# Performance work log

Measured on AMD Instinct MI355X. Metric: run time of the kernel, lower is better.

The kernel has to match this reference:

```python
import jax, jax.numpy as jnp
from jax import lax
import numpy as np

D_MODEL = 512
D_STATE = 16
D_CONV = 4
EXPAND = 2
D_INNER = EXPAND * D_MODEL
DT_RANK = (D_MODEL + 15) // 16  # ceil(d_model/16) = 32
B, L = 4, 1024


def setup_inputs() -> dict:
    key = jax.random.key(0)
    ks = jax.random.split(key, 12)
    s = 0.02
    inp = {
        "feature": jax.random.normal(ks[0], (B, L, D_MODEL), jnp.float32),
        "ln_w": jnp.ones((D_MODEL,), jnp.float32),
        "ln_b": jnp.zeros((D_MODEL,), jnp.float32),
        "in_proj_w": jax.random.normal(ks[1], (2 * D_INNER, D_MODEL), jnp.float32) * s,
        "conv_w": jax.random.normal(ks[2], (D_INNER, D_CONV), jnp.float32) * 0.1,
        "conv_b": jnp.zeros((D_INNER,), jnp.float32),
        "x_proj_w": jax.random.normal(ks[3], (DT_RANK + 2 * D_STATE, D_INNER), jnp.float32) * s,
        "dt_proj_w": jax.random.normal(ks[4], (D_INNER, DT_RANK), jnp.float32) * 0.1,
        "dt_proj_b": jax.random.normal(ks[5], (D_INNER,), jnp.float32) * 0.1 - 4.0,
        "A_log": jnp.log(jnp.broadcast_to(jnp.arange(1, D_STATE + 1, dtype=jnp.float32), (D_INNER, D_STATE))),
        "D": jnp.ones((D_INNER,), jnp.float32),
        "out_proj_w": jax.random.normal(ks[6], (D_MODEL, D_INNER), jnp.float32) * s,
    }
    return inp


def _mamba_block(xn, in_proj_w, conv_w, conv_b, x_proj_w, dt_proj_w, dt_proj_b, A_log, D, out_proj_w):
    # xn: [B, L, d_model]
    xz = jnp.einsum('bld,ed->ble', xn, in_proj_w)          # [B, L, 2*d_inner]
    x, z = xz[..., :D_INNER], xz[..., D_INNER:]
    # causal depthwise conv along L
    xc = jnp.transpose(x, (0, 2, 1))                        # [B, d_inner, L]
    xc = lax.conv_general_dilated(
        xc, conv_w[:, None, :], (1,), [(D_CONV - 1, 0)],
        feature_group_count=D_INNER,
        dimension_numbers=('NCH', 'OIH', 'NCH')) + conv_b[None, :, None]
    x = jax.nn.silu(jnp.transpose(xc, (0, 2, 1)))           # [B, L, d_inner]
    x_dbl = jnp.einsum('bld,ed->ble', x, x_proj_w)          # [B, L, dt_rank+2*d_state]
    dt = x_dbl[..., :DT_RANK]
    Bm = x_dbl[..., DT_RANK:DT_RANK + D_STATE]
    Cm = x_dbl[..., DT_RANK + D_STATE:]
    dt = jax.nn.softplus(jnp.einsum('blr,dr->bld', dt, dt_proj_w) + dt_proj_b)  # [B,L,d_inner]
    A = -jnp.exp(A_log)                                     # [d_inner, d_state]

    def step(h, inp):
        dt_t, B_t, C_t, x_t = inp                           # [B,d_inner],[B,d_state],[B,d_state],[B,d_inner]
        dA = jnp.exp(dt_t[..., None] * A)                   # [B, d_inner, d_state]
        h = dA * h + (dt_t * x_t)[..., None] * B_t[:, None, :]
        y = jnp.einsum('bds,bs->bd', h, C_t)
        return h, y

    xs = (jnp.transpose(dt, (1, 0, 2)), jnp.transpose(Bm, (1, 0, 2)),
          jnp.transpose(Cm, (1, 0, 2)), jnp.transpose(x, (1, 0, 2)))
    h0 = jnp.zeros((xn.shape[0], D_INNER, D_STATE), xn.dtype)
    _, ys = lax.scan(step, h0, xs)                          # ys: [L, B, d_inner]
    y = jnp.transpose(ys, (1, 0, 2)) + x * D
    y = y * jax.nn.silu(z)
    return jnp.einsum('bld,ed->ble', y, out_proj_w)         # [B, L, d_model]


def reference(feature, ln_w, ln_b, in_proj_w, conv_w, conv_b, x_proj_w,
              dt_proj_w, dt_proj_b, A_log, D, out_proj_w):
    eps = 1e-5
    mu = jnp.mean(feature, axis=-1, keepdims=True)
    var = jnp.var(feature, axis=-1, keepdims=True)
    xn = (feature - mu) / jnp.sqrt(var + eps) * ln_w + ln_b
    out = _mamba_block(xn, in_proj_w, conv_w, conv_b, x_proj_w,
                       dt_proj_w, dt_proj_b, A_log, D, out_proj_w)
    return xn + out
```

## Files before the change

kernel.cpp:

```cpp
#include <hip/hip_runtime.h>
#include <hip/hip_bf16.h>
#include <math.h>

#define B_SZ 4
#define L_SZ 1024
#define DM   512
#define DI   1024
#define DS   16
#define DTR  32
#define NXD  64
#define M_ROWS (B_SZ*L_SZ)
#define CHK  64
#define CLEN 16
#define NCH  (B_SZ*DI)
#define PLANE (NCH*DS)
#define LDA  40
#define KSPL 8

typedef __attribute__((ext_vector_type(8))) short short8;
typedef __attribute__((ext_vector_type(4))) float f32x4;
typedef __hip_bfloat16 bf16;

__device__ __forceinline__ float bf2f(bf16 x){ return __bfloat162float(x); }
__device__ __forceinline__ float fsig(float x){ return __builtin_amdgcn_rcpf(1.f + __expf(-x)); }
__device__ __forceinline__ unsigned short bfbits(float x){ bf16 b = __float2bfloat16(x); return *(unsigned short*)&b; }
#define LOG2E 1.44269504f

__device__ __forceinline__ bool is_f32(const void* lnw){
    return *(const unsigned*)lnw == 0x3F800000u;
}
__device__ __forceinline__ float loadf(const void* s, int i, bool f){
    return f ? ((const float*)s)[i] : bf2f(((const bf16*)s)[i]);
}
__device__ __forceinline__ bf16 loadb(const void* s, int i, bool f){
    return f ? __float2bfloat16(((const float*)s)[i]) : ((const bf16*)s)[i];
}

#define CVT_TOTAL 1694720
__global__ __launch_bounds__(256) void prep_kernel(
        const void* __restrict__ feat, const void* __restrict__ lnw, const void* __restrict__ lnb,
        const void* __restrict__ w_in, const void* __restrict__ w_x, const void* __restrict__ w_out,
        const void* __restrict__ w_dt, const void* __restrict__ b_dt,
        const void* __restrict__ alog, const void* __restrict__ dvec,
        const void* __restrict__ cw, const void* __restrict__ cb,
        bf16* __restrict__ WINB, bf16* __restrict__ WXB, bf16* __restrict__ WOUTB,
        float* __restrict__ WDTT, float* __restrict__ BDT, float* __restrict__ ALOG,
        float* __restrict__ DVEC, float* __restrict__ CWF, float* __restrict__ CBF,
        bf16* __restrict__ xnb, float* __restrict__ XDBL) {
    bool f = is_f32(lnw);
    if (blockIdx.y == 0) {
        int id = blockIdx.x*256 + threadIdx.x;
        if (id < M_ROWS*NXD) XDBL[id] = 0.f;
        #pragma unroll 2
        for (int g = id; g < CVT_TOTAL; g += 1048576) {
            if      (g < 1048576)  WINB[g] = loadb(w_in, g, f);
            else if (g < 1114112)  WXB[g-1048576] = loadb(w_x, g-1048576, f);
            else if (g < 1638400)  WOUTB[g-1114112] = loadb(w_out, g-1114112, f);
            else if (g < 1671168){ int i = g-1638400; WDTT[(i&(DTR-1))*DI + (i>>5)] = loadf(w_dt, i, f); }
            else if (g < 1672192)  BDT[g-1671168] = loadf(b_dt, g-1671168, f);
            else if (g < 1688576)  ALOG[g-1672192] = loadf(alog, g-1672192, f);
            else if (g < 1689600)  DVEC[g-1688576] = loadf(dvec, g-1688576, f);
            else if (g < 1693696)  CWF[g-1689600] = loadf(cw, g-1689600, f);
            else                   CBF[g-1693696] = loadf(cb, g-1693696, f);
        }
    } else {
        int row = blockIdx.x;
        int t = threadIdx.x;
        size_t base = (size_t)row*DM;
        float v0 = loadf(feat, base+t, f);
        float v1 = loadf(feat, base+t+256, f);
        __shared__ float ssum[256], ssq[256];
        ssum[t] = v0+v1; ssq[t] = v0*v0+v1*v1;
        __syncthreads();
        for (int off=128; off>0; off>>=1){
            if (t<off){ ssum[t]+=ssum[t+off]; ssq[t]+=ssq[t+off]; }
            __syncthreads();
        }
        float mu  = ssum[0]*(1.0f/DM);
        float var = ssq[0]*(1.0f/DM) - mu*mu;
        float rstd = rsqrtf(var + 1e-5f);
        float o0 = (v0-mu)*rstd*loadf(lnw,t,f)     + loadf(lnb,t,f);
        float o1 = (v1-mu)*rstd*loadf(lnw,t+256,f) + loadf(lnb,t+256,f);
        xnb[base + t]     = __float2bfloat16(o0);
        xnb[base + t+256] = __float2bfloat16(o1);
    }
}


__global__ __launch_bounds__(256) void gemm_in_mfma(const bf16* __restrict__ A,
        const bf16* __restrict__ W, bf16* __restrict__ XB, bf16* __restrict__ ZB) {
    const int K = 512;
    __shared__ bf16 As[128*LDA];
    __shared__ bf16 Bs[128*LDA];
    int t = threadIdx.x;
    int w = t>>6, l = t&63;
    int wm = w&1, wn = w>>1;
    int row0 = blockIdx.y*128, col0 = blockIdx.x*128;
    int lr = l&15, lq = l>>4;
    int srow = t>>2, scol = (t&3)*8;
    const bf16* pA0 = A + (size_t)(row0+srow)*K    + scol;
    const bf16* pA1 = A + (size_t)(row0+64+srow)*K + scol;
    const bf16* pB0 = W + (size_t)(col0+srow)*K    + scol;
    const bf16* pB1 = W + (size_t)(col0+64+srow)*K + scol;
    f32x4 acc[4][4] = {};
    short8 a0 = *(const short8*)(pA0);
    short8 a1 = *(const short8*)(pA1);
    short8 b0 = *(const short8*)(pB0);
    short8 b1 = *(const short8*)(pB1);
    for (int k0=0; k0<K; k0+=32) {
        __syncthreads();
        *(short8*)(As + srow*LDA + scol)      = a0;
        *(short8*)(As + (64+srow)*LDA + scol) = a1;
        *(short8*)(Bs + srow*LDA + scol)      = b0;
        *(short8*)(Bs + (64+srow)*LDA + scol) = b1;
        __syncthreads();
        if (k0 + 32 < K) {
            a0 = *(const short8*)(pA0 + k0 + 32);
            a1 = *(const short8*)(pA1 + k0 + 32);
            b0 = *(const short8*)(pB0 + k0 + 32);
            b1 = *(const short8*)(pB1 + k0 + 32);
        }
        short8 af[4], bfr[4];
        #pragma unroll
        for (int mi=0;mi<4;mi++) af[mi]  = *(const short8*)(As + (wm*64+mi*16+lr)*LDA + lq*8);
        #pragma unroll
        for (int ni=0;ni<4;ni++) bfr[ni] = *(const short8*)(Bs + (wn*64+ni*16+lr)*LDA + lq*8);
        #pragma unroll
        for (int mi=0;mi<4;mi++)
            #pragma unroll
            for (int ni=0;ni<4;ni++)
                acc[mi][ni] = __builtin_amdgcn_mfma_f32_16x16x32_bf16(af[mi], bfr[ni], acc[mi][ni], 0,0,0);
    }
    bf16* dst; int cbn;
    if (col0 < DI) { dst = XB; cbn = col0; } else { dst = ZB; cbn = col0 - DI; }
    #pragma unroll
    for (int mi=0;mi<4;mi++)
        #pragma unroll
        for (int ni=0;ni<4;ni++) {
            int r = row0 + wm*64 + mi*16 + lq*4;
            int c = cbn  + wn*64 + ni*16 + lr;
            #pragma unroll
            for (int rr=0;rr<4;rr++)
                dst[(size_t)(r+rr)*DI + c] = __float2bfloat16(acc[mi][ni][rr]);
        }
}

__global__ __launch_bounds__(256) void gemm_xc_mfma(const bf16* __restrict__ XB,
        const bf16* __restrict__ W, const float* __restrict__ cw, const float* __restrict__ cb,
        bf16* __restrict__ XC, float* __restrict__ C) {
    const int K = 1024;
    __shared__ bf16 As[64*LDA];
    __shared__ bf16 Bs[64*LDA];
    int t = threadIdx.x;
    int w = t>>6, l64 = t&63;
    int wm = w&1, wn = w>>1;
    int row0 = blockIdx.y*64;
    int kbeg = blockIdx.x*(K/KSPL), kend = kbeg + K/KSPL;
    int lr = l64&15, lq = l64>>4;
    int srow = t>>2, scol = (t&3)*8;
    int m = row0 + srow;
    int lpos = m & (L_SZ-1);
    bool vr0 = lpos >= 3, vr1 = lpos >= 2, vr2 = lpos >= 1;
    const bf16* pxb = XB + (size_t)(m-3)*DI + kbeg + scol;
    const bf16* pB0 = W + (size_t)srow*K + kbeg + scol;
    f32x4 acc[2][2] = {};
    short8 x0 = *(const short8*)(pxb);
    short8 x1 = *(const short8*)(pxb + DI);
    short8 x2 = *(const short8*)(pxb + 2*DI);
    short8 x3 = *(const short8*)(pxb + 3*DI);
    short8 b0 = *(const short8*)(pB0);
    for (int k0=kbeg; k0<kend; k0+=32) {
        int dbase = k0 + scol;
        short8 xx0 = x0, xx1 = x1, xx2 = x2;
        if (!vr0) xx0 = (short8){0,0,0,0,0,0,0,0};
        if (!vr1) xx1 = (short8){0,0,0,0,0,0,0,0};
        if (!vr2) xx2 = (short8){0,0,0,0,0,0,0,0};
        uint a0[4], a1[4], a2[4], a3[4];
        *(uint4*)a0 = *(uint4*)&xx0; *(uint4*)a1 = *(uint4*)&xx1;
        *(uint4*)a2 = *(uint4*)&xx2; *(uint4*)a3 = *(uint4*)&x3;
        uint outw[4];
        #pragma unroll
        for (int jw=0; jw<4; jw++){
            float r2[2];
            #pragma unroll
            for (int hi=0; hi<2; hi++){
                int dch = dbase + jw*2 + hi;
                float4 wv = *(const float4*)(cw + (size_t)dch*4);
                float accv = cb[dch];
                float e0 = hi ? __uint_as_float(a0[jw] & 0xffff0000u) : __uint_as_float(a0[jw] << 16);
                float e1 = hi ? __uint_as_float(a1[jw] & 0xffff0000u) : __uint_as_float(a1[jw] << 16);
                float e2 = hi ? __uint_as_float(a2[jw] & 0xffff0000u) : __uint_as_float(a2[jw] << 16);
                float e3 = hi ? __uint_as_float(a3[jw] & 0xffff0000u) : __uint_as_float(a3[jw] << 16);
                accv = fmaf(e0, wv.x, accv); accv = fmaf(e1, wv.y, accv);
                accv = fmaf(e2, wv.z, accv); accv = fmaf(e3, wv.w, accv);
                r2[hi] = accv * fsig(accv);
            }
            outw[jw] = (uint)bfbits(r2[0]) | ((uint)bfbits(r2[1]) << 16);
        }
        short8 cv; *(uint4*)&cv = *(uint4*)outw;
        __syncthreads();
        *(short8*)(As + srow*LDA + scol) = cv;
        *(short8*)(Bs + srow*LDA + scol) = b0;
        __syncthreads();
        *(short8*)(XC + (size_t)m*DI + dbase) = cv;
        if (k0 + 32 < kend) {
            pxb += 32; pB0 += 32;
            x0 = *(const short8*)(pxb);
            x1 = *(const short8*)(pxb + DI);
            x2 = *(const short8*)(pxb + 2*DI);
            x3 = *(const short8*)(pxb + 3*DI);
            b0 = *(const short8*)(pB0);
        }
        short8 af[2], bfr[2];
        #pragma unroll
        for (int mi=0;mi<2;mi++) af[mi]  = *(const short8*)(As + (wm*32+mi*16+lr)*LDA + lq*8);
        #pragma unroll
        for (int ni=0;ni<2;ni++) bfr[ni] = *(const short8*)(Bs + (wn*32+ni*16+lr)*LDA + lq*8);
        #pragma unroll
        for (int mi=0;mi<2;mi++)
            #pragma unroll
            for (int ni=0;ni<2;ni++)
                acc[mi][ni] = __builtin_amdgcn_mfma_f32_16x16x32_bf16(af[mi], bfr[ni], acc[mi][ni], 0,0,0);
    }
    #pragma unroll
    for (int mi=0;mi<2;mi++)
        #pragma unroll
        for (int ni=0;ni<2;ni++) {
            int r = row0 + wm*32 + mi*16 + lq*4;
            int c = wn*32 + ni*16 + lr;
            #pragma unroll
            for (int rr=0;rr<4;rr++)
                atomicAdd(&C[(size_t)(r+rr)*NXD + c], acc[mi][ni][rr]);
        }
}

__global__ __launch_bounds__(256) void gemm_out_mfma(const bf16* __restrict__ A,
        const bf16* __restrict__ W, const bf16* __restrict__ xnb,
        void* __restrict__ out, const void* __restrict__ lnw) {
    const int K = 1024;
    __shared__ bf16 As[128*LDA];
    __shared__ bf16 Bs[64*LDA];
    int t = threadIdx.x;
    int w = t>>6, l = t&63;
    int wm = w&1, wn = w>>1;
    int row0 = blockIdx.y*128, col0 = blockIdx.x*64;
    int lr = l&15, lq = l>>4;
    int srow = t>>2, scol = (t&3)*8;
    const bf16* pA0 = A + (size_t)(row0+srow)*K    + scol;
    const bf16* pA1 = A + (size_t)(row0+64+srow)*K + scol;
    const bf16* pB0 = W + (size_t)(col0+srow)*K    + scol;
    f32x4 acc[4][2] = {};
    short8 a0 = *(const short8*)(pA0);
    short8 a1 = *(const short8*)(pA1);
    short8 b0 = *(const short8*)(pB0);
    for (int k0=0; k0<K; k0+=32) {
        __syncthreads();
        *(short8*)(As + srow*LDA + scol)      = a0;
        *(short8*)(As + (64+srow)*LDA + scol) = a1;
        *(short8*)(Bs + srow*LDA + scol)      = b0;
        __syncthreads();
        if (k0 + 32 < K) {
            a0 = *(const short8*)(pA0 + k0 + 32);
            a1 = *(const short8*)(pA1 + k0 + 32);
            b0 = *(const short8*)(pB0 + k0 + 32);
        }
        short8 af[4], bfr[2];
        #pragma unroll
        for (int mi=0;mi<4;mi++) af[mi]  = *(const short8*)(As + (wm*64+mi*16+lr)*LDA + lq*8);
        #pragma unroll
        for (int ni=0;ni<2;ni++) bfr[ni] = *(const short8*)(Bs + (wn*32+ni*16+lr)*LDA + lq*8);
        #pragma unroll
        for (int mi=0;mi<4;mi++)
            #pragma unroll
            for (int ni=0;ni<2;ni++)
                acc[mi][ni] = __builtin_amdgcn_mfma_f32_16x16x32_bf16(af[mi], bfr[ni], acc[mi][ni], 0,0,0);
    }
    bool f = is_f32(lnw);
    #pragma unroll
    for (int mi=0;mi<4;mi++)
        #pragma unroll
        for (int ni=0;ni<2;ni++) {
            int r = row0 + wm*64 + mi*16 + lq*4;
            int c = col0 + wn*32 + ni*16 + lr;
            #pragma unroll
            for (int rr=0;rr<4;rr++) {
                float v = acc[mi][ni][rr] + bf2f(xnb[(size_t)(r+rr)*DM + c]);
                if (f) ((float*)out)[(size_t)(r+rr)*DM + c] = v;
                else   ((bf16*)out)[(size_t)(r+rr)*DM + c] = __float2bfloat16(v);
            }
        }
}


__global__ __launch_bounds__(256) void scan_p1(const bf16* __restrict__ xc,
        const float* __restrict__ xdbl, const float* __restrict__ dtwT,
        const float* __restrict__ dtb, const float* __restrict__ A_log,
        bf16* __restrict__ SP, bf16* __restrict__ PP) {
    int ch = blockIdx.x*256 + threadIdx.x;
    int j  = blockIdx.y;
    int d  = ch & (DI-1);
    int bu = __builtin_amdgcn_readfirstlane(ch >> 10);
    float a2[DS];
    {
        const float4* pa = (const float4*)(A_log + d*DS);
        #pragma unroll
        for (int q=0;q<4;q++){
            float4 v = pa[q];
            a2[q*4+0] = -__expf(v.x)*LOG2E; a2[q*4+1] = -__expf(v.y)*LOG2E;
            a2[q*4+2] = -__expf(v.z)*LOG2E; a2[q*4+3] = -__expf(v.w)*LOG2E;
        }
    }
    float wdt[DTR];
    #pragma unroll
    for (int r=0;r<DTR;r++) wdt[r] = dtwT[r*DI + d];
    float bias = dtb[d];
    float h[DS], P[DS];
    #pragma unroll
    for (int s=0;s<DS;s++){ h[s]=0.f; P[s]=1.f; }
    size_t row = (size_t)bu*L_SZ + (size_t)j*CLEN;
    const bf16* pxc = xc  + row*DI + d;
    const float* pX = xdbl + row*NXD;
    #pragma unroll 2
    for (int t=0; t<CLEN; t++) {
        float acc = bias;
        #pragma unroll
        for (int r=0;r<DTR;r++) acc = fmaf(pX[r], wdt[r], acc);
        float dt = (acc > 20.f) ? acc : __logf(1.f + __expf(acc));
        float u  = dt * bf2f(*pxc);
        const float* pB = pX + DTR;
        #pragma unroll
        for (int s=0;s<DS;s++){
            float dA = __builtin_exp2f(dt*a2[s]);
            h[s] = fmaf(dA, h[s], u*pB[s]);
            P[s] *= dA;
        }
        pxc += DI; pX += NXD;
    }
    bf16* sp = SP + (size_t)j*PLANE + ch;
    bf16* pp = PP + (size_t)j*PLANE + ch;
    #pragma unroll
    for (int s=0;s<DS;s++){ sp[s*NCH] = __float2bfloat16(h[s]); pp[s*NCH] = __float2bfloat16(P[s]); }
}

__global__ void scan_p2(const bf16* __restrict__ SP, const bf16* __restrict__ PP,
                        bf16* __restrict__ HB) {
    int idx = blockIdx.x*256 + threadIdx.x;
    float H = 0.f;
    for (int j=0;j<CHK;j++){
        size_t o = (size_t)j*PLANE + idx;
        float p = bf2f(PP[o]), s = bf2f(SP[o]);
        HB[o] = __float2bfloat16(H);
        H = fmaf(p, H, s);
    }
}

__global__ __launch_bounds__(256) void scan_p3(const bf16* __restrict__ xc,
        const float* __restrict__ xdbl, const float* __restrict__ dtwT,
        const float* __restrict__ dtb, const float* __restrict__ A_log,
        const float* __restrict__ Dp, const bf16* __restrict__ HB,
        const bf16* __restrict__ zb, bf16* __restrict__ ybf) {
    int ch = blockIdx.x*256 + threadIdx.x;
    int j  = blockIdx.y;
    int d  = ch & (DI-1);
    int bu = __builtin_amdgcn_readfirstlane(ch >> 10);
    float a2[DS];
    {
        const float4* pa = (const float4*)(A_log + d*DS);
        #pragma unroll
        for (int q=0;q<4;q++){
            float4 v = pa[q];
            a2[q*4+0] = -__expf(v.x)*LOG2E; a2[q*4+1] = -__expf(v.y)*LOG2E;
            a2[q*4+2] = -__expf(v.z)*LOG2E; a2[q*4+3] = -__expf(v.w)*LOG2E;
        }
    }
    float wdt[DTR];
    #pragma unroll
    for (int r=0;r<DTR;r++) wdt[r] = dtwT[r*DI + d];
    float bias = dtb[d];
    float h[DS];
    {
        const bf16* ph = HB + (size_t)j*PLANE + ch;
        #pragma unroll
        for (int s=0;s<DS;s++) h[s] = bf2f(ph[s*NCH]);
    }
    float Dd = Dp[d];
    size_t row = (size_t)bu*L_SZ + (size_t)j*CLEN;
    const bf16* pxc = xc  + row*DI + d;
    const float* pX = xdbl + row*NXD;
    const bf16* pz  = zb  + row*DI + d;
    bf16*       py  = ybf + row*DI + d;
    #pragma unroll 2
    for (int t=0; t<CLEN; t++) {
        float acc = bias;
        #pragma unroll
        for (int r=0;r<DTR;r++) acc = fmaf(pX[r], wdt[r], acc);
        float dt = (acc > 20.f) ? acc : __logf(1.f + __expf(acc));
        float xv = bf2f(*pxc);
        float u  = dt * xv;
        const float* pB = pX + DTR;
        const float* pC = pX + DTR + DS;
        float y0=0.f, y1=0.f, y2=0.f, y3=0.f;
        #pragma unroll
        for (int s=0;s<DS;s+=4){
            float dA0 = __builtin_exp2f(dt*a2[s]);
            float dA1 = __builtin_exp2f(dt*a2[s+1]);
            float dA2 = __builtin_exp2f(dt*a2[s+2]);
            float dA3 = __builtin_exp2f(dt*a2[s+3]);
            h[s]   = fmaf(dA0, h[s],   u*pB[s]);
            h[s+1] = fmaf(dA1, h[s+1], u*pB[s+1]);
            h[s+2] = fmaf(dA2, h[s+2], u*pB[s+2]);
            h[s+3] = fmaf(dA3, h[s+3], u*pB[s+3]);
            y0 = fmaf(h[s],   pC[s],   y0);
            y1 = fmaf(h[s+1], pC[s+1], y1);
            y2 = fmaf(h[s+2], pC[s+2], y2);
            y3 = fmaf(h[s+3], pC[s+3], y3);
        }
        float y = (y0+y1) + (y2+y3) + xv*Dd;
        float z = bf2f(*pz);
        *py = __float2bfloat16(y * z * fsig(z));
        pxc += DI; pX += NXD; pz += DI; py += DI;
    }
}

extern "C" void kernel_launch(void* const* d_in, const int* in_sizes, int n_in,
                              void* d_out, int out_size, void* d_ws, size_t ws_size,
                              hipStream_t stream) {
    float* FW = (float*)d_ws;
    bf16*  SPB  = (bf16*)FW;
    bf16*  PPB  = (bf16*)(FW + 2097152);
    bf16*  HBB  = (bf16*)(FW + 4194304);
    bf16*  XNB  = (bf16*)(FW + 6291456);
    float* XDBL = FW + 7340032;
    float* WDTT = FW + 7602176;
    float* BDT  = FW + 7634944;
    float* ALOG = FW + 7635968;
    float* DVEC = FW + 7652352;
    float* CWF  = FW + 7653376;
    float* CBF  = FW + 7657472;
    bf16* XBB  = (bf16*)(FW + 7658496);
    bf16* YBF  = XBB;
    bf16* ZBB  = (bf16*)(FW + 9755648);
    bf16* XCB  = (bf16*)(FW + 11852800);
    bf16* WINB = (bf16*)(FW + 13949952);
    bf16* WXB  = (bf16*)(FW + 14474240);
    bf16* WOUTB= (bf16*)(FW + 14507008);

    prep_kernel<<<dim3(4096, 2), 256, 0, stream>>>(
        d_in[0], d_in[1], d_in[2], d_in[3], d_in[6], d_in[11], d_in[7], d_in[8],
        d_in[9], d_in[10], d_in[4], d_in[5],
        WINB, WXB, WOUTB, WDTT, BDT, ALOG, DVEC, CWF, CBF, XNB, XDBL);
    gemm_in_mfma<<<dim3(2048/128, M_ROWS/128), 256, 0, stream>>>(XNB, WINB, XBB, ZBB);
    gemm_xc_mfma<<<dim3(KSPL, M_ROWS/64), 256, 0, stream>>>(XBB, WXB, CWF, CBF, XCB, XDBL);
    scan_p1<<<dim3(NCH/256, CHK), 256, 0, stream>>>(XCB, XDBL, WDTT, BDT, ALOG, SPB, PPB);
    scan_p2<<<PLANE/256, 256, 0, stream>>>(SPB, PPB, HBB);
    scan_p3<<<dim3(NCH/256, CHK), 256, 0, stream>>>(XCB, XDBL, WDTT, BDT, ALOG, DVEC, HBB, ZBB, YBF);
    gemm_out_mfma<<<dim3(DM/64, M_ROWS/128), 256, 0, stream>>>(YBF, WOUTB, XNB, d_out, d_in[1]);
}
```

Before: 209.6 us.

## Use direct global-to-LDS async loads with double buffering in input/output GEMMs

Replaces the register-staged global-to-shared copies in the input and output projection GEMMs with global_load_lds 16-byte direct loads into double-buffered LDS tiles. An XOR swizzle on the column chunk replaces the padded LDA layout to avoid bank conflicts. The aim is to drop one barrier per k-step, free registers, and overlap the next tile's fetch with the current MFMA work. It relies on the compiler placing a vmcnt wait before the barrier so that the async LDS writes are visible in time.

Result: no change. 209.4 us (median of 2 runs) (-0.1%).

```diff
diff --git a/kernel.cpp b/kernel.cpp
--- a/kernel.cpp
+++ b/kernel.cpp
@@ -25,6 +25,12 @@
 __device__ __forceinline__ float fsig(float x){ return __builtin_amdgcn_rcpf(1.f + __expf(-x)); }
 __device__ __forceinline__ unsigned short bfbits(float x){ bf16 b = __float2bfloat16(x); return *(unsigned short*)&b; }
 #define LOG2E 1.44269504f
+
+typedef __attribute__((address_space(1))) const unsigned gu32;
+typedef __attribute__((address_space(3))) unsigned lu32;
+__device__ __forceinline__ void gload16(const void* g, void* l) {
+    __builtin_amdgcn_global_load_lds((gu32*)g, (lu32*)l, 16, 0, 0);
+}
 
 __device__ __forceinline__ bool is_f32(const void* lnw){
     return *(const unsigned*)lnw == 0x3F800000u;
@@ -90,41 +96,44 @@
 __global__ __launch_bounds__(256) void gemm_in_mfma(const bf16* __restrict__ A,
         const bf16* __restrict__ W, bf16* __restrict__ XB, bf16* __restrict__ ZB) {
     const int K = 512;
-    __shared__ bf16 As[128*LDA];
-    __shared__ bf16 Bs[128*LDA];
+    __shared__ bf16 As[2][128*32];
+    __shared__ bf16 Bs[2][128*32];
     int t = threadIdx.x;
     int w = t>>6, l = t&63;
     int wm = w&1, wn = w>>1;
     int row0 = blockIdx.y*128, col0 = blockIdx.x*128;
     int lr = l&15, lq = l>>4;
-    int srow = t>>2, scol = (t&3)*8;
-    const bf16* pA0 = A + (size_t)(row0+srow)*K    + scol;
-    const bf16* pA1 = A + (size_t)(row0+64+srow)*K + scol;
-    const bf16* pB0 = W + (size_t)(col0+srow)*K    + scol;
-    const bf16* pB1 = W + (size_t)(col0+64+srow)*K + scol;
+    int r0 = t>>2,        c0 = (t&3) ^ ((r0>>1)&3);
+    int i1 = 256 + t;
+    int r1 = i1>>2,       c1 = (i1&3) ^ ((r1>>1)&3);
+    const bf16* gA0 = A + (size_t)(row0+r0)*K + c0*8;
+    const bf16* gA1 = A + (size_t)(row0+r1)*K + c1*8;
+    const bf16* gB0 = W + (size_t)(col0+r0)*K + c0*8;
+    const bf16* gB1 = W + (size_t)(col0+r1)*K + c1*8;
+    int coff = ((lq ^ ((lr>>1)&3)))*8;
+    int aoff = (wm*64+lr)*32 + coff;
+    int boff = (wn*64+lr)*32 + coff;
     f32x4 acc[4][4] = {};
-    short8 a0 = *(const short8*)(pA0);
-    short8 a1 = *(const short8*)(pA1);
-    short8 b0 = *(const short8*)(pB0);
-    short8 b1 = *(const short8*)(pB1);
-    for (int k0=0; k0<K; k0+=32) {
+    gload16(gA0, &As[0][t*8]);
+    gload16(gA1, &As[0][i1*8]);
+    gload16(gB0, &Bs[0][t*8]);
+    gload16(gB1, &Bs[0][i1*8]);
+    const int NK = K/32;
+    for (int kt=0; kt<NK; kt++) {
+        int cur = kt&1;
         __syncthreads();
-        *(short8*)(As + srow*LDA + scol)      = a0;
-        *(short8*)(As + (64+srow)*LDA + scol) = a1;
-        *(short8*)(Bs + srow*LDA + scol)      = b0;
-        *(short8*)(Bs + (64+srow)*LDA + scol) = b1;
-        __syncthreads();
-        if (k0 + 32 < K) {
-            a0 = *(const short8*)(pA0 + k0 + 32);
-            a1 = *(const short8*)(pA1 + k0 + 32);
-            b0 = *(const short8*)(pB0 + k0 + 32);
-            b1 = *(const short8*)(pB1 + k0 + 32);
+        if (kt+1 < NK) {
+            int nxt = cur^1, ko = (kt+1)*32;
+            gload16(gA0 + ko, &As[nxt][t*8]);
+            gload16(gA1 + ko, &As[nxt][i1*8]);
+            gload16(gB0 + ko, &Bs[nxt][t*8]);
+            gload16(gB1 + ko, &Bs[nxt][i1*8]);
         }
         short8 af[4], bfr[4];
         #pragma unroll
-        for (int mi=0;mi<4;mi++) af[mi]  = *(const short8*)(As + (wm*64+mi*16+lr)*LDA + lq*8);
-        #pragma unroll
-        for (int ni=0;ni<4;ni++) bfr[ni] = *(const short8*)(Bs + (wn*64+ni*16+lr)*LDA + lq*8);
+        for (int mi=0;mi<4;mi++) af[mi]  = *(const short8*)(&As[cur][aoff + mi*512]);
+        #pragma unroll
+        for (int ni=0;ni<4;ni++) bfr[ni] = *(const short8*)(&Bs[cur][boff + ni*512]);
         #pragma unroll
         for (int mi=0;mi<4;mi++)
             #pragma unroll
@@ -238,37 +247,41 @@
         const bf16* __restrict__ W, const bf16* __restrict__ xnb,
         void* __restrict__ out, const void* __restrict__ lnw) {
     const int K = 1024;
-    __shared__ bf16 As[128*LDA];
-    __shared__ bf16 Bs[64*LDA];
+    __shared__ bf16 As[2][128*32];
+    __shared__ bf16 Bs[2][64*32];
     int t = threadIdx.x;
     int w = t>>6, l = t&63;
     int wm = w&1, wn = w>>1;
     int row0 = blockIdx.y*128, col0 = blockIdx.x*64;
     int lr = l&15, lq = l>>4;
-    int srow = t>>2, scol = (t&3)*8;
-    const bf16* pA0 = A + (size_t)(row0+srow)*K    + scol;
-    const bf16* pA1 = A + (size_t)(row0+64+srow)*K + scol;
-    const bf16* pB0 = W + (size_t)(col0+srow)*K    + scol;
+    int r0 = t>>2,  c0 = (t&3) ^ ((r0>>1)&3);
+    int i1 = 256 + t;
+    int r1 = i1>>2, c1 = (i1&3) ^ ((r1>>1)&3);
+    const bf16* gA0 = A + (size_t)(row0+r0)*K + c0*8;
+    const bf16* gA1 = A + (size_t)(row0+r1)*K + c1*8;
+    const bf16* gB0 = W + (size_t)(col0+r0)*K + c0*8;
+    int coff = ((lq ^ ((lr>>1)&3)))*8;
+    int aoff = (wm*64+lr)*32 + coff;
+    int boff = (wn*32+lr)*32 + coff;
     f32x4 acc[4][2] = {};
-    short8 a0 = *(const short8*)(pA0);
-    short8 a1 = *(const short8*)(pA1);
-    short8 b0 = *(const short8*)(pB0);
-    for (int k0=0; k0<K; k0+=32) {
+    gload16(gA0, &As[0][t*8]);
+    gload16(gA1, &As[0][i1*8]);
+    gload16(gB0, &Bs[0][t*8]);
+    const int NK = K/32;
+    for (int kt=0; kt<NK; kt++) {
+        int cur = kt&1;
         __syncthreads();
-        *(short8*)(As + srow*LDA + scol)      = a0;
-        *(short8*)(As + (64+srow)*LDA + scol) = a1;
-        *(short8*)(Bs + srow*LDA + scol)      = b0;
-        __syncthreads();
-        if (k0 + 32 < K) {
-            a0 = *(const short8*)(pA0 + k0 + 32);
-            a1 = *(const short8*)(pA1 + k0 + 32);
-            b0 = *(const short8*)(pB0 + k0 + 32);
+        if (kt+1 < NK) {
+            int nxt = cur^1, ko = (kt+1)*32;
+            gload16(gA0 + ko, &As[nxt][t*8]);
+            gload16(gA1 + ko, &As[nxt][i1*8]);
+            gload16(gB0 + ko, &Bs[nxt][t*8]);
         }
         short8 af[4], bfr[2];
         #pragma unroll
-        for (int mi=0;mi<4;mi++) af[mi]  = *(const short8*)(As + (wm*64+mi*16+lr)*LDA + lq*8);
-        #pragma unroll
-        for (int ni=0;ni<2;ni++) bfr[ni] = *(const short8*)(Bs + (wn*32+ni*16+lr)*LDA + lq*8);
+        for (int mi=0;mi<4;mi++) af[mi]  = *(const short8*)(&As[cur][aoff + mi*512]);
+        #pragma unroll
+        for (int ni=0;ni<2;ni++) bfr[ni] = *(const short8*)(&Bs[cur][boff + ni*512]);
         #pragma unroll
         for (int mi=0;mi<4;mi++)
             #pragma unroll
```
